# Kernel tuning notes

Measured on AMD Instinct MI355X. Metric: run time of the kernel, lower is better.

Reference implementation:

```python
import jax, jax.numpy as jnp
import numpy as np

N = 50000
E = 600000
D = 128
EPS = 1e-5  # nn.LayerNorm default eps


def gcn_conv(x, W, b, src, dst):
    # PyG GCNConv with add_self_loops=True, edge_weight=None (all ones),
    # symmetric normalization D^-1/2 (A+I) D^-1/2.
    h = x @ W                                        # [N, D]
    deg = jnp.zeros((N,), h.dtype).at[dst].add(1.0) + 1.0  # +1 for self loop
    dinv = jax.lax.rsqrt(deg)                        # deg >= 1, safe
    norm = dinv[src] * dinv[dst]                     # [E]
    msg = h[src] * norm[:, None]                     # [E, D] gather
    agg = jax.ops.segment_sum(msg, dst, num_segments=N)
    agg = agg + h * (dinv * dinv)[:, None]           # self-loop term
    return agg + b


def layer_norm(x, g, b):
    mu = jnp.mean(x, axis=-1, keepdims=True)
    var = jnp.mean(jnp.square(x - mu), axis=-1, keepdims=True)
    return (x - mu) * jax.lax.rsqrt(var + EPS) * g + b


def setup_inputs() -> dict:
    key = jax.random.key(0)
    ks = jax.random.split(key, 6)
    x = jax.random.normal(ks[0], (N, D), dtype=jnp.float32)
    edge_index = jax.random.randint(ks[1], (2, E), 0, N, dtype=jnp.int64)
    s = 1.0 / np.sqrt(D)
    W1 = jax.random.uniform(ks[2], (D, D), jnp.float32, -s, s)
    W2 = jax.random.uniform(ks[3], (D, D), jnp.float32, -s, s)
    b1 = jnp.zeros((D,), jnp.float32)
    b2 = jnp.zeros((D,), jnp.float32)
    ln1_g = jnp.ones((D,), jnp.float32)
    ln1_b = jnp.zeros((D,), jnp.float32)
    ln2_g = jnp.ones((D,), jnp.float32)
    ln2_b = jnp.zeros((D,), jnp.float32)
    return {"x": x, "edge_index": edge_index, "W1": W1, "b1": b1,
            "ln1_g": ln1_g, "ln1_b": ln1_b, "W2": W2, "b2": b2,
            "ln2_g": ln2_g, "ln2_b": ln2_b}


def reference(x, edge_index, W1, b1, ln1_g, ln1_b, W2, b2, ln2_g, ln2_b):
    src, dst = edge_index[0], edge_index[1]
    out = gcn_conv(x, W1, b1, src, dst)
    out = jax.nn.relu(layer_norm(out, ln1_g, ln1_b))  # dropout = identity (eval)
    out = gcn_conv(out, W2, b2, src, dst)
    out = jax.nn.relu(layer_norm(out, ln2_g, ln2_b))
    return out + x
```

## Files before the change

kernel.cpp:

```cpp
#include <hip/hip_runtime.h>
#include <hip/hip_fp16.h>

#define D 128
#define EPS 1e-5f
#define KB 64
#define NBSH 7
#define BUCKW 128

typedef unsigned int u32;
typedef unsigned short u16;
typedef unsigned char u8;
typedef __attribute__((ext_vector_type(8))) _Float16 half8;
typedef __attribute__((ext_vector_type(4))) float f32x4;
typedef __attribute__((ext_vector_type(2))) float f32x2;

__device__ inline u16 f2h(float x) {
  _Float16 t = (_Float16)x;
  return __builtin_bit_cast(u16, t);
}
__device__ inline u8 f2fp8(float x) {
  return (u8)(__builtin_amdgcn_cvt_pk_fp8_f32(x, x, 0, false) & 0xff);
}

__global__ __launch_bounds__(256) void k_prep(const float* __restrict__ W1,
                                              const float* __restrict__ W2,
                                              u16* __restrict__ Wt1,
                                              u16* __restrict__ Wt2) {
  int i = blockIdx.x * 256 + threadIdx.x;
  if (i < 2 * D * D) {
    const float* W = (i < D * D) ? W1 : W2;
    u16* Wt = (i < D * D) ? Wt1 : Wt2;
    int ii = i & (D * D - 1);
    int k = ii >> 7, c = ii & 127;
    Wt[c * D + k] = f2h(W[ii]);
  }
}

template <bool F32IN>
__device__ __forceinline__ void gemm_body(const void* __restrict__ in_,
                                          const u16* __restrict__ Wt,
                                          u8* __restrict__ out, int nrows,
                                          int blk) {
  const int tid = threadIdx.x;
  const int lane = tid & 63, wv = tid >> 6;
  const int m = lane & 15, q = lane >> 4;
  const int r0 = blk * 64 + wv * 16;
  const int rowa = min(r0 + m, nrows - 1);

  f32x4 acc[8];
#pragma unroll
  for (int ct = 0; ct < 8; ct++) acc[ct] = (f32x4)(0.0f);

#pragma unroll
  for (int kk = 0; kk < 4; kk++) {
    const int kbase = kk * 32 + q * 8;
    half8 a;
    if (F32IN) {
      const float* in = (const float*)in_;
      float4 v0 = *(const float4*)(in + (size_t)rowa * D + kbase);
      float4 v1 = *(const float4*)(in + (size_t)rowa * D + kbase + 4);
      a[0] = (_Float16)v0.x; a[1] = (_Float16)v0.y;
      a[2] = (_Float16)v0.z; a[3] = (_Float16)v0.w;
      a[4] = (_Float16)v1.x; a[5] = (_Float16)v1.y;
      a[6] = (_Float16)v1.z; a[7] = (_Float16)v1.w;
    } else {
      const u16* in = (const u16*)in_;
      a = *(const half8*)(in + (size_t)rowa * D + kbase);
    }
#pragma unroll
    for (int ct = 0; ct < 8; ct++) {
      half8 b = *(const half8*)(Wt + (ct * 16 + m) * D + kbase);
      acc[ct] = __builtin_amdgcn_mfma_f32_16x16x32_f16(a, b, acc[ct], 0, 0, 0);
    }
  }

#pragma unroll
  for (int ct = 0; ct < 8; ct++) {
#pragma unroll
    for (int rg = 0; rg < 4; rg++) {
      int rr = r0 + q * 4 + rg;
      if (rr < nrows) out[(size_t)rr * D + ct * 16 + m] = f2fp8(acc[ct][rg]);
    }
  }
}

__global__ __launch_bounds__(256) void k_count_gemm1(
    const int* __restrict__ dst, int* __restrict__ cnt, int E, int NB, int EPB,
    const float* __restrict__ x, const u16* __restrict__ Wt1,
    u8* __restrict__ A, int nrows) {
  if (blockIdx.x < (u32)KB) {
    __shared__ int hist[512];
    const int k = blockIdx.x, tid = threadIdx.x;
    for (int i = tid; i < NB; i += 256) hist[i] = 0;
    __syncthreads();
    const int e0 = k * EPB, e1 = min(E, e0 + EPB);
    for (int base = e0 + tid; base < e1; base += 2048) {
      int dd[8];
#pragma unroll
      for (int i = 0; i < 8; i++) {
        int e = base + i * 256;
        dd[i] = (e < e1) ? dst[e] : -1;
      }
#pragma unroll
      for (int i = 0; i < 8; i++)
        if (dd[i] >= 0) atomicAdd(&hist[dd[i] >> NBSH], 1);
    }
    __syncthreads();
    for (int b = tid; b < NB; b += 256) cnt[b * KB + k] = hist[b];
  } else {
    gemm_body<true>(x, Wt1, A, nrows, blockIdx.x - KB);
  }
}

__global__ __launch_bounds__(256) void k_scan_reduce(
    const int* __restrict__ cnt, int M, int* __restrict__ bsum) {
  const int b = blockIdx.x, t = threadIdx.x;
  const int lane = t & 63, w = t >> 6;
  int idx = b * 1024 + t * 4;
  int4 v = make_int4(0, 0, 0, 0);
  if (idx + 3 < M) {
    v = *(const int4*)(cnt + idx);
  } else {
    if (idx + 0 < M) v.x = cnt[idx + 0];
    if (idx + 1 < M) v.y = cnt[idx + 1];
    if (idx + 2 < M) v.z = cnt[idx + 2];
  }
  int s = v.x + v.y + v.z + v.w;
#pragma unroll
  for (int o = 1; o < 64; o <<= 1) s += __shfl_xor(s, o, 64);
  __shared__ int ws[4];
  if (lane == 0) ws[w] = s;
  __syncthreads();
  if (t == 0) bsum[b] = ws[0] + ws[1] + ws[2] + ws[3];
}

__global__ __launch_bounds__(64) void k_scan_mid(const int* __restrict__ bsum,
                                                 int* __restrict__ boff,
                                                 int SB, int* __restrict__ bsv,
                                                 int NB, int E) {
  const int lane = threadIdx.x;
  int running = 0;
  for (int base = 0; base < SB; base += 64) {
    int i = base + lane;
    int v = (i < SB) ? bsum[i] : 0;
    int incl = v;
#pragma unroll
    for (int o = 1; o < 64; o <<= 1) {
      int t = __shfl_up(incl, o, 64);
      if (lane >= o) incl += t;
    }
    if (i < SB) boff[i] = running + incl - v;
    running += __shfl(incl, 63, 64);
  }
  if (lane == 0) bsv[NB] = E;
}

__global__ __launch_bounds__(256) void k_scan_apply(
    int* __restrict__ cnt, int M, const int* __restrict__ boff,
    int* __restrict__ bsv) {
  const int b = blockIdx.x, t = threadIdx.x;
  const int lane = t & 63, w = t >> 6;
  int idx = b * 1024 + t * 4;
  int4 v = make_int4(0, 0, 0, 0);
  if (idx + 3 < M) {
    v = *(const int4*)(cnt + idx);
  } else {
    if (idx + 0 < M) v.x = cnt[idx + 0];
    if (idx + 1 < M) v.y = cnt[idx + 1];
    if (idx + 2 < M) v.z = cnt[idx + 2];
  }
  int s = v.x + v.y + v.z + v.w;
  int incl = s;
#pragma unroll
  for (int o = 1; o < 64; o <<= 1) {
    int u = __shfl_up(incl, o, 64);
    if (lane >= o) incl += u;
  }
  __shared__ int ws[4];
  if (lane == 63) ws[w] = incl;
  __syncthreads();
  int wbase = 0;
#pragma unroll
  for (int j = 0; j < 4; j++)
    if (j < w) wbase += ws[j];
  int base = boff[b] + wbase + incl - s;
  int e0 = base, e1 = e0 + v.x, e2 = e1 + v.y, e3 = e2 + v.z;
  if (idx < M) {
    cnt[idx] = e0;
    if ((idx & (KB - 1)) == 0) bsv[idx >> 6] = e0;
  }
  if (idx + 1 < M) cnt[idx + 1] = e1;
  if (idx + 2 < M) cnt[idx + 2] = e2;
  if (idx + 3 < M) cnt[idx + 3] = e3;
}

__global__ __launch_bounds__(256) void k_scatter(
    const int* __restrict__ src, const int* __restrict__ dst,
    const int* __restrict__ cnt, u32* __restrict__ tmp, int E, int NB,
    int EPB) {
  __shared__ int off[512];
  const int k = blockIdx.x, tid = threadIdx.x;
  for (int b = tid; b < NB; b += 256) off[b] = cnt[b * KB + k];
  __syncthreads();
  const int e0 = k * EPB, e1 = min(E, e0 + EPB);
  for (int base = e0 + tid; base < e1; base += 2048) {
    int dd[8], ss[8];
#pragma unroll
    for (int i = 0; i < 8; i++) {
      int e = base + i * 256;
      dd[i] = (e < e1) ? dst[e] : -1;
      ss[i] = (e < e1) ? src[e] : 0;
    }
#pragma unroll
    for (int i = 0; i < 8; i++) {
      if (dd[i] >= 0) {
        int p = atomicAdd(&off[dd[i] >> NBSH], 1);
        tmp[p] = (u32)ss[i] | ((u32)(dd[i] & (BUCKW - 1)) << 16);
      }
    }
  }
}

__global__ __launch_bounds__(256) void k_bucket(
    const u32* __restrict__ tmp, const int* __restrict__ bsv,
    int4* __restrict__ meta, float* __restrict__ dinv,
    u32* __restrict__ csr, int N) {
  __shared__ int hist[BUCKW];
  __shared__ int sc[BUCKW];
  __shared__ int cur[BUCKW];
  const int b = blockIdx.x, tid = threadIdx.x;
  const int s0 = bsv[b], s1 = bsv[b + 1];
  if (tid < BUCKW) hist[tid] = 0;
  __syncthreads();
  for (int base = s0 + tid; base < s1; base += 1024) {
    int tt[4];
#pragma unroll
    for (int i = 0; i < 4; i++) {
      int idx = base + i * 256;
      tt[i] = (idx < s1) ? (int)tmp[idx] : -1;
    }
#pragma unroll
    for (int i = 0; i < 4; i++)
      if (tt[i] >= 0) atomicAdd(&hist[(tt[i] >> 16) & (BUCKW - 1)], 1);
  }
  __syncthreads();
  if (tid < BUCKW) sc[tid] = hist[tid];
  __syncthreads();
#pragma unroll
  for (int o = 1; o < BUCKW; o <<= 1) {
    int t = 0;
    if (tid < BUCKW && tid >= o) t = sc[tid - o];
    __syncthreads();
    if (tid < BUCKW) sc[tid] += t;
    __syncthreads();
  }
  if (tid < BUCKW) {
    int dg = hist[tid];
    int excl = sc[tid] - dg;
    cur[tid] = excl;
    int d = (b << NBSH) + tid;
    if (d < N) {
      float dv = rsqrtf((float)dg + 1.0f);
      meta[d] = make_int4(s0 + excl, dg, __builtin_bit_cast(int, dv), 0);
      dinv[d] = dv;
    }
  }
  __syncthreads();
  for (int base = s0 + tid; base < s1; base += 1024) {
    int tt[4];
#pragma unroll
    for (int i = 0; i < 4; i++) {
      int idx = base + i * 256;
      tt[i] = (idx < s1) ? (int)tmp[idx] : -1;
    }
#pragma unroll
    for (int i = 0; i < 4; i++) {
      if (tt[i] >= 0) {
        int r = atomicAdd(&cur[(tt[i] >> 16) & (BUCKW - 1)], 1);
        csr[s0 + r] = (u32)tt[i] & 0xffffu;
      }
    }
  }
}

__global__ __launch_bounds__(256) void k_weights(
    const int4* __restrict__ meta, const float* __restrict__ dinv,
    u32* __restrict__ csr, int N) {
  int gid = blockIdx.x * 256 + threadIdx.x;
  int r = gid >> 2, j0 = gid & 3;
  if (r >= N) return;
  int4 mt = meta[r];
  float dv = __builtin_bit_cast(float, mt.z);
  for (int j = j0; j < mt.y; j += 4) {
    u32 s = csr[mt.x + j];
    float w = dinv[s] * dv;
    csr[mt.x + j] = s | ((u32)f2h(w) << 16);
  }
}

#define ACC_EDGE(vv, ee)                                                     \
  {                                                                          \
    float ww = (float)__builtin_bit_cast(_Float16, (u16)((ee) >> 16));       \
    f32x2 p_;                                                                \
    p_ = __builtin_amdgcn_cvt_pk_f32_fp8(vv.x, false);                       \
    acc[0] = fmaf(p_[0], ww, acc[0]); acc[1] = fmaf(p_[1], ww, acc[1]);      \
    p_ = __builtin_amdgcn_cvt_pk_f32_fp8(vv.x, true);                        \
    acc[2] = fmaf(p_[0], ww, acc[2]); acc[3] = fmaf(p_[1], ww, acc[3]);      \
    p_ = __builtin_amdgcn_cvt_pk_f32_fp8(vv.y, false);                       \
    acc[4] = fmaf(p_[0], ww, acc[4]); acc[5] = fmaf(p_[1], ww, acc[5]);      \
    p_ = __builtin_amdgcn_cvt_pk_f32_fp8(vv.y, true);                        \
    acc[6] = fmaf(p_[0], ww, acc[6]); acc[7] = fmaf(p_[1], ww, acc[7]);      \
  }

__device__ __forceinline__ void gather_ln_core(
    const uint2* __restrict__ hb, const int4* __restrict__ meta,
    const u32* __restrict__ csr, const float* __restrict__ b,
    const float* __restrict__ g, const float* __restrict__ bln,
    int row, int n, int sl, float out[8]) {
  const bool valid = row < n;
  const int rc = valid ? row : 0;
  int4 mt = meta[rc];
  int beg = mt.x;
  int cnt = valid ? mt.y : 0;
  float dv = __builtin_bit_cast(float, mt.z);
  float sn = dv * dv;

  float acc[8];
  {
    uint2 su = hb[(size_t)rc * 16 + sl];
    f32x2 p0 = __builtin_amdgcn_cvt_pk_f32_fp8(su.x, false);
    f32x2 p1 = __builtin_amdgcn_cvt_pk_f32_fp8(su.x, true);
    f32x2 p2 = __builtin_amdgcn_cvt_pk_f32_fp8(su.y, false);
    f32x2 p3 = __builtin_amdgcn_cvt_pk_f32_fp8(su.y, true);
    acc[0] = p0[0] * sn; acc[1] = p0[1] * sn;
    acc[2] = p1[0] * sn; acc[3] = p1[1] * sn;
    acc[4] = p2[0] * sn; acc[5] = p2[1] * sn;
    acc[6] = p3[0] * sn; acc[7] = p3[1] * sn;
  }

  int cm = max(cnt, __shfl_xor(cnt, 16, 64));
  cm = max(cm, __shfl_xor(cm, 32, 64));

  for (int j0 = 0; j0 < cm; j0 += 8) {
    u32 e[8];
#pragma unroll
    for (int jj = 0; jj < 8; jj++) {
      int j = j0 + jj;
      e[jj] = (j < cnt) ? csr[beg + j] : 0u;
    }
    uint2 v[8];
#pragma unroll
    for (int jj = 0; jj < 8; jj++)
      v[jj] = hb[(size_t)(e[jj] & 0xffffu) * 16 + sl];
#pragma unroll
    for (int jj = 0; jj < 8; jj++) ACC_EDGE(v[jj], e[jj]);
  }

  int d0 = sl * 8;
  float4 bb0 = *(const float4*)(b + d0);
  float4 bb1 = *(const float4*)(b + d0 + 4);
  float a0 = acc[0] + bb0.x, a1 = acc[1] + bb0.y;
  float a2 = acc[2] + bb0.z, a3 = acc[3] + bb0.w;
  float a4 = acc[4] + bb1.x, a5 = acc[5] + bb1.y;
  float a6 = acc[6] + bb1.z, a7 = acc[7] + bb1.w;

  float sum = ((a0 + a1) + (a2 + a3)) + ((a4 + a5) + (a6 + a7));
#pragma unroll
  for (int o = 8; o >= 1; o >>= 1) sum += __shfl_xor(sum, o, 16);
  float mu = sum * (1.0f / 128.0f);
  float e0 = a0 - mu, e1 = a1 - mu, e2 = a2 - mu, e3 = a3 - mu;
  float e4 = a4 - mu, e5 = a5 - mu, e6 = a6 - mu, e7 = a7 - mu;
  float vs = ((e0 * e0 + e1 * e1) + (e2 * e2 + e3 * e3)) +
             ((e4 * e4 + e5 * e5) + (e6 * e6 + e7 * e7));
#pragma unroll
  for (int o = 8; o >= 1; o >>= 1) vs += __shfl_xor(vs, o, 16);
  float inv = rsqrtf(vs * (1.0f / 128.0f) + EPS);

  float4 gg0 = *(const float4*)(g + d0);
  float4 gg1 = *(const float4*)(g + d0 + 4);
  float4 bl0 = *(const float4*)(bln + d0);
  float4 bl1 = *(const float4*)(bln + d0 + 4);
  out[0] = fmaxf(e0 * inv * gg0.x + bl0.x, 0.0f);
  out[1] = fmaxf(e1 * inv * gg0.y + bl0.y, 0.0f);
  out[2] = fmaxf(e2 * inv * gg0.z + bl0.z, 0.0f);
  out[3] = fmaxf(e3 * inv * gg0.w + bl0.w, 0.0f);
  out[4] = fmaxf(e4 * inv * gg1.x + bl1.x, 0.0f);
  out[5] = fmaxf(e5 * inv * gg1.y + bl1.y, 0.0f);
  out[6] = fmaxf(e6 * inv * gg1.z + bl1.z, 0.0f);
  out[7] = fmaxf(e7 * inv * gg1.w + bl1.w, 0.0f);
}

__global__ __launch_bounds__(256, 8) void k_gather1(
    const uint2* __restrict__ hb, const int4* __restrict__ meta,
    const u32* __restrict__ csr,
    const float* __restrict__ b, const float* __restrict__ g,
    const float* __restrict__ bln,
    u16* __restrict__ y1, int n) {
  const int tid = threadIdx.x;
  const int sl = tid & 15;
  const int row = blockIdx.x * 16 + (tid >> 4);
  float o[8];
  gather_ln_core(hb, meta, csr, b, g, bln, row, n, sl, o);
  if (row >= n) return;
  uint4 pk;
  pk.x = ((u32)f2h(o[1]) << 16) | (u32)f2h(o[0]);
  pk.y = ((u32)f2h(o[3]) << 16) | (u32)f2h(o[2]);
  pk.z = ((u32)f2h(o[5]) << 16) | (u32)f2h(o[4]);
  pk.w = ((u32)f2h(o[7]) << 16) | (u32)f2h(o[6]);
  *(uint4*)(y1 + (size_t)row * D + sl * 8) = pk;
}

__global__ __launch_bounds__(256) void k_gemm2(const u16* __restrict__ y1,
                                               const u16* __restrict__ Wt2,
                                               u8* __restrict__ outB, int n) {
  gemm_body<false>(y1, Wt2, outB, n, blockIdx.x);
}

__global__ __launch_bounds__(256, 8) void k_gather2(
    const uint2* __restrict__ hb, const int4* __restrict__ meta,
    const u32* __restrict__ csr,
    const float* __restrict__ b, const float* __restrict__ g,
    const float* __restrict__ bln, const float* __restrict__ resid,
    float* __restrict__ outf, int n) {
  const int tid = threadIdx.x;
  const int sl = tid & 15;
  const int row = blockIdx.x * 16 + (tid >> 4);
  float o[8];
  gather_ln_core(hb, meta, csr, b, g, bln, row, n, sl, o);
  if (row >= n) return;
  size_t base = (size_t)row * D + sl * 8;
  float4 r0 = *(const float4*)(resid + base);
  float4 r1 = *(const float4*)(resid + base + 4);
  *(float4*)(outf + base) =
      make_float4(o[0] + r0.x, o[1] + r0.y, o[2] + r0.z, o[3] + r0.w);
  *(float4*)(outf + base + 4) =
      make_float4(o[4] + r1.x, o[5] + r1.y, o[6] + r1.z, o[7] + r1.w);
}

extern "C" void kernel_launch(void* const* d_in, const int* in_sizes, int n_in,
                              void* d_out, int out_size, void* d_ws, size_t ws_size,
                              hipStream_t stream) {
  const float* x    = (const float*)d_in[0];
  const int*   ei   = (const int*)d_in[1];
  const float* W1   = (const float*)d_in[2];
  const float* b1   = (const float*)d_in[3];
  const float* g1   = (const float*)d_in[4];
  const float* bl1  = (const float*)d_in[5];
  const float* W2   = (const float*)d_in[6];
  const float* b2   = (const float*)d_in[7];
  const float* g2   = (const float*)d_in[8];
  const float* bl2  = (const float*)d_in[9];

  const int N = in_sizes[0] / D;
  const int E = in_sizes[1] / 2;
  const int* src = ei;
  const int* dst = ei + E;

  const int NB  = (N + BUCKW - 1) / BUCKW;
  const int M   = NB * KB;
  const int EPB = (E + KB - 1) / KB;
  const int GB  = (N + 63) / 64;
  const int RB  = (N + 15) / 16;
  const int SB  = (M + 1023) / 1024;

  size_t off = 0;
  auto walloc = [&](size_t bytes) {
    void* p = (char*)d_ws + off;
    off = (off + bytes + 255) & ~(size_t)255;
    return p;
  };
  int*   cnt   = (int*)walloc((size_t)M * 4);
  int*   bsum  = (int*)walloc((size_t)SB * 4);
  int*   boff  = (int*)walloc((size_t)SB * 4);
  int*   bsv   = (int*)walloc((size_t)(NB + 1) * 4);
  u32*   tmp   = (u32*)walloc((size_t)E * 4);
  u32*   csr   = (u32*)walloc((size_t)E * 4);
  int4*  meta  = (int4*)walloc((size_t)N * 16);
  float* dinv  = (float*)walloc((size_t)N * 4);
  u8*    A     = (u8*)walloc((size_t)N * D);
  u8*    B     = (u8*)walloc((size_t)N * D);
  u16*   Wt1   = (u16*)walloc((size_t)D * D * 2);
  u16*   Wt2   = (u16*)walloc((size_t)D * D * 2);
  u16*   y1    = (u16*)walloc((size_t)N * D * 2);
  float* O     = (float*)d_out;

  k_prep<<<(2 * D * D + 255) / 256, 256, 0, stream>>>(W1, W2, Wt1, Wt2);
  k_count_gemm1<<<KB + GB, 256, 0, stream>>>(dst, cnt, E, NB, EPB, x, Wt1, A, N);
  k_scan_reduce<<<SB, 256, 0, stream>>>(cnt, M, bsum);
  k_scan_mid<<<1, 64, 0, stream>>>(bsum, boff, SB, bsv, NB, E);
  k_scan_apply<<<SB, 256, 0, stream>>>(cnt, M, boff, bsv);
  k_scatter<<<KB, 256, 0, stream>>>(src, dst, cnt, tmp, E, NB, EPB);
  k_bucket<<<NB, 256, 0, stream>>>(tmp, bsv, meta, dinv, csr, N);
  k_weights<<<(N * 4 + 255) / 256, 256, 0, stream>>>(meta, dinv, csr, N);
  k_gather1<<<RB, 256, 0, stream>>>((const uint2*)A, meta, csr, b1, g1, bl1,
                                    y1, N);
  k_gemm2<<<GB, 256, 0, stream>>>(y1, Wt2, B, N);
  k_gather2<<<RB, 256, 0, stream>>>((const uint2*)B, meta, csr,
                                    b2, g2, bl2, x, O, N);
}
```

Baseline: 193.8 us.

## Compute degrees early, fold edge weights into bucket pass, drop scan_mid and weights kernels

Per-node degrees are now counted with global atomics during the histogram pass, and dinv is computed alongside the scan reduce. This lets the bucket kernel write normalized fp16 edge weights directly into the CSR, removing the separate k_weights pass. The single-block scan_mid kernel is removed by having each scan_apply block sum the preceding block totals itself. The gather loop also prefetches the next batch of CSR entries. The cost is 600k extra global atomics on deg and redundant prefix summation in each scan_apply block, in exchange for two fewer launches and one fewer CSR read-modify-write pass.

New measurement: 205.7 us. 1.06x slower.

```diff
diff --git a/kernel.cpp b/kernel.cpp
--- a/kernel.cpp
+++ b/kernel.cpp
@@ -25,14 +25,18 @@
 __global__ __launch_bounds__(256) void k_prep(const float* __restrict__ W1,
                                               const float* __restrict__ W2,
                                               u16* __restrict__ Wt1,
-                                              u16* __restrict__ Wt2) {
-  int i = blockIdx.x * 256 + threadIdx.x;
-  if (i < 2 * D * D) {
+                                              u16* __restrict__ Wt2,
+                                              int* __restrict__ deg, int N) {
+  if (blockIdx.x < 128) {
+    int i = blockIdx.x * 256 + threadIdx.x;
     const float* W = (i < D * D) ? W1 : W2;
     u16* Wt = (i < D * D) ? Wt1 : Wt2;
     int ii = i & (D * D - 1);
     int k = ii >> 7, c = ii & 127;
     Wt[c * D + k] = f2h(W[ii]);
+  } else {
+    int i = (blockIdx.x - 128) * 256 + threadIdx.x;
+    if (i < N) deg[i] = 0;
   }
 }
 
@@ -85,7 +89,8 @@
 }
 
 __global__ __launch_bounds__(256) void k_count_gemm1(
-    const int* __restrict__ dst, int* __restrict__ cnt, int E, int NB, int EPB,
+    const int* __restrict__ dst, int* __restrict__ cnt, int* __restrict__ deg,
+    int E, int NB, int EPB,
     const float* __restrict__ x, const u16* __restrict__ Wt1,
     u8* __restrict__ A, int nrows) {
   if (blockIdx.x < (u32)KB) {
@@ -103,7 +108,10 @@
       }
 #pragma unroll
       for (int i = 0; i < 8; i++)
-        if (dd[i] >= 0) atomicAdd(&hist[dd[i] >> NBSH], 1);
+        if (dd[i] >= 0) {
+          atomicAdd(&hist[dd[i] >> NBSH], 1);
+          atomicAdd(&deg[dd[i]], 1);
+        }
     }
     __syncthreads();
     for (int b = tid; b < NB; b += 256) cnt[b * KB + k] = hist[b];
@@ -113,7 +121,15 @@
 }
 
 __global__ __launch_bounds__(256) void k_scan_reduce(
-    const int* __restrict__ cnt, int M, int* __restrict__ bsum) {
+    const int* __restrict__ cnt, int M, int* __restrict__ bsum,
+    const int* __restrict__ deg, float* __restrict__ dinv, int N, int SB,
+    int* __restrict__ bsv, int NB, int E) {
+  if ((int)blockIdx.x >= SB) {
+    int i = ((int)blockIdx.x - SB) * 256 + threadIdx.x;
+    if (i < N) dinv[i] = rsqrtf((float)deg[i] + 1.0f);
+    if ((int)blockIdx.x == SB && threadIdx.x == 0) bsv[NB] = E;
+    return;
+  }
   const int b = blockIdx.x, t = threadIdx.x;
   const int lane = t & 63, w = t >> 6;
   int idx = b * 1024 + t * 4;
@@ -134,29 +150,8 @@
   if (t == 0) bsum[b] = ws[0] + ws[1] + ws[2] + ws[3];
 }
 
-__global__ __launch_bounds__(64) void k_scan_mid(const int* __restrict__ bsum,
-                                                 int* __restrict__ boff,
-                                                 int SB, int* __restrict__ bsv,
-                                                 int NB, int E) {
-  const int lane = threadIdx.x;
-  int running = 0;
-  for (int base = 0; base < SB; base += 64) {
-    int i = base + lane;
-    int v = (i < SB) ? bsum[i] : 0;
-    int incl = v;
-#pragma unroll
-    for (int o = 1; o < 64; o <<= 1) {
-      int t = __shfl_up(incl, o, 64);
-      if (lane >= o) incl += t;
-    }
-    if (i < SB) boff[i] = running + incl - v;
-    running += __shfl(incl, 63, 64);
-  }
-  if (lane == 0) bsv[NB] = E;
-}
-
 __global__ __launch_bounds__(256) void k_scan_apply(
-    int* __restrict__ cnt, int M, const int* __restrict__ boff,
+    int* __restrict__ cnt, int M, const int* __restrict__ bsum,
     int* __restrict__ bsv) {
   const int b = blockIdx.x, t = threadIdx.x;
   const int lane = t & 63, w = t >> 6;
@@ -177,13 +172,21 @@
     if (lane >= o) incl += u;
   }
   __shared__ int ws[4];
+  __shared__ int sboff;
   if (lane == 63) ws[w] = incl;
+  if (t < 64) {
+    int partial = 0;
+    for (int j = t; j < b; j += 64) partial += bsum[j];
+#pragma unroll
+    for (int o = 32; o >= 1; o >>= 1) partial += __shfl_xor(partial, o, 64);
+    if (t == 0) sboff = partial;
+  }
   __syncthreads();
   int wbase = 0;
 #pragma unroll
   for (int j = 0; j < 4; j++)
     if (j < w) wbase += ws[j];
-  int base = boff[b] + wbase + incl - s;
+  int base = sboff + wbase + incl - s;
   int e0 = base, e1 = e0 + v.x, e2 = e1 + v.y, e3 = e2 + v.z;
   if (idx < M) {
     cnt[idx] = e0;
@@ -223,14 +226,19 @@
 
 __global__ __launch_bounds__(256) void k_bucket(
     const u32* __restrict__ tmp, const int* __restrict__ bsv,
-    int4* __restrict__ meta, float* __restrict__ dinv,
+    const float* __restrict__ dinv, int4* __restrict__ meta,
     u32* __restrict__ csr, int N) {
   __shared__ int hist[BUCKW];
   __shared__ int sc[BUCKW];
   __shared__ int cur[BUCKW];
+  __shared__ float sdv[BUCKW];
   const int b = blockIdx.x, tid = threadIdx.x;
   const int s0 = bsv[b], s1 = bsv[b + 1];
-  if (tid < BUCKW) hist[tid] = 0;
+  if (tid < BUCKW) {
+    hist[tid] = 0;
+    int d = (b << NBSH) + tid;
+    sdv[tid] = (d < N) ? dinv[d] : 0.0f;
+  }
   __syncthreads();
   for (int base = s0 + tid; base < s1; base += 1024) {
     int tt[4];
@@ -259,11 +267,8 @@
     int excl = sc[tid] - dg;
     cur[tid] = excl;
     int d = (b << NBSH) + tid;
-    if (d < N) {
-      float dv = rsqrtf((float)dg + 1.0f);
-      meta[d] = make_int4(s0 + excl, dg, __builtin_bit_cast(int, dv), 0);
-      dinv[d] = dv;
-    }
+    if (d < N)
+      meta[d] = make_int4(s0 + excl, dg, __builtin_bit_cast(int, sdv[tid]), 0);
   }
   __syncthreads();
   for (int base = s0 + tid; base < s1; base += 1024) {
@@ -273,28 +278,19 @@
       int idx = base + i * 256;
       tt[i] = (idx < s1) ? (int)tmp[idx] : -1;
     }
+    float wsrc[4];
+#pragma unroll
+    for (int i = 0; i < 4; i++)
+      wsrc[i] = (tt[i] >= 0) ? dinv[(u32)tt[i] & 0xffffu] : 0.0f;
 #pragma unroll
     for (int i = 0; i < 4; i++) {
       if (tt[i] >= 0) {
-        int r = atomicAdd(&cur[(tt[i] >> 16) & (BUCKW - 1)], 1);
-        csr[s0 + r] = (u32)tt[i] & 0xffffu;
+        int dl = (tt[i] >> 16) & (BUCKW - 1);
+        int r = atomicAdd(&cur[dl], 1);
+        csr[s0 + r] =
+            ((u32)tt[i] & 0xffffu) | ((u32)f2h(wsrc[i] * sdv[dl]) << 16);
       }
     }
-  }
-}
-
-__global__ __launch_bounds__(256) void k_weights(
-    const int4* __restrict__ meta, const float* __restrict__ dinv,
-    u32* __restrict__ csr, int N) {
-  int gid = blockIdx.x * 256 + threadIdx.x;
-  int r = gid >> 2, j0 = gid & 3;
-  if (r >= N) return;
-  int4 mt = meta[r];
-  float dv = __builtin_bit_cast(float, mt.z);
-  for (int j = j0; j < mt.y; j += 4) {
-    u32 s = csr[mt.x + j];
-    float w = dinv[s] * dv;
-    csr[mt.x + j] = s | ((u32)f2h(w) << 16);
   }
 }
 
@@ -341,19 +337,25 @@
   int cm = max(cnt, __shfl_xor(cnt, 16, 64));
   cm = max(cm, __shfl_xor(cm, 32, 64));
 
+  u32 e[8];
+#pragma unroll
+  for (int jj = 0; jj < 8; jj++)
+    e[jj] = (jj < cnt) ? csr[beg + jj] : 0u;
+
   for (int j0 = 0; j0 < cm; j0 += 8) {
-    u32 e[8];
-#pragma unroll
-    for (int jj = 0; jj < 8; jj++) {
-      int j = j0 + jj;
-      e[jj] = (j < cnt) ? csr[beg + j] : 0u;
-    }
     uint2 v[8];
 #pragma unroll
     for (int jj = 0; jj < 8; jj++)
       v[jj] = hb[(size_t)(e[jj] & 0xffffu) * 16 + sl];
+    u32 en[8];
+    const int jn = j0 + 8;
+#pragma unroll
+    for (int jj = 0; jj < 8; jj++)
+      en[jj] = (jn + jj < cnt) ? csr[beg + jn + jj] : 0u;
 #pragma unroll
     for (int jj = 0; jj < 8; jj++) ACC_EDGE(v[jj], e[jj]);
+#pragma unroll
+    for (int jj = 0; jj < 8; jj++) e[jj] = en[jj];
   }
 
   int d0 = sl * 8;
@@ -462,6 +464,7 @@
   const int GB  = (N + 63) / 64;
   const int RB  = (N + 15) / 16;
   const int SB  = (M + 1023) / 1024;
+  const int ZB  = (N + 255) / 256;
 
   size_t off = 0;
   auto walloc = [&](size_t bytes) {
@@ -471,8 +474,8 @@
   };
   int*   cnt   = (int*)walloc((size_t)M * 4);
   int*   bsum  = (int*)walloc((size_t)SB * 4);
-  int*   boff  = (int*)walloc((size_t)SB * 4);
   int*   bsv   = (int*)walloc((size_t)(NB + 1) * 4);
+  int*   deg   = (int*)walloc((size_t)N * 4);
   u32*   tmp   = (u32*)walloc((size_t)E * 4);
   u32*   csr   = (u32*)walloc((size_t)E * 4);
   int4*  meta  = (int4*)walloc((size_t)N * 16);
@@ -484,14 +487,14 @@
   u16*   y1    = (u16*)walloc((size_t)N * D * 2);
   float* O     = (float*)d_out;
 
-  k_prep<<<(2 * D * D + 255) / 256, 256, 0, stream>>>(W1, W2, Wt1, Wt2);
-  k_count_gemm1<<<KB + GB, 256, 0, stream>>>(dst, cnt, E, NB, EPB, x, Wt1, A, N);
-  k_scan_reduce<<<SB, 256, 0, stream>>>(cnt, M, bsum);
-  k_scan_mid<<<1, 64, 0, stream>>>(bsum, boff, SB, bsv, NB, E);
-  k_scan_apply<<<SB, 256, 0, stream>>>(cnt, M, boff, bsv);
+  k_prep<<<128 + ZB, 256, 0, stream>>>(W1, W2, Wt1, Wt2, deg, N);
+  k_count_gemm1<<<KB + GB, 256, 0, stream>>>(dst, cnt, deg, E, NB, EPB,
+                                             x, Wt1, A, N);
+  k_scan_reduce<<<SB + ZB, 256, 0, stream>>>(cnt, M, bsum, deg, dinv, N, SB,
+                                             bsv, NB, E);
+  k_scan_apply<<<SB, 256, 0, stream>>>(cnt, M, bsum, bsv);
   k_scatter<<<KB, 256, 0, stream>>>(src, dst, cnt, tmp, E, NB, EPB);
-  k_bucket<<<NB, 256, 0, stream>>>(tmp, bsv, meta, dinv, csr, N);
-  k_weights<<<(N * 4 + 255) / 256, 256, 0, stream>>>(meta, dinv, csr, N);
+  k_bucket<<<NB, 256, 0, stream>>>(tmp, bsv, dinv, meta, csr, N);
   k_gather1<<<RB, 256, 0, stream>>>((const uint2*)A, meta, csr, b1, g1, bl1,
                                     y1, N);
   k_gemm2<<<GB, 256, 0, stream>>>(y1, Wt2, B, N);
```

## Sort rows by degree for gather load balance and fold scan-mid into scan-apply

Applied to the files above, without the earlier changes.

Builds a degree histogram in the bucket kernel, scans it, and writes a degree-sorted row permutation in the weights kernel. Both gather kernels now process rows in that order, so the 16 rows sharing a block have similar edge counts and lanes diverge less. Separately, the single-block mid-scan kernel is removed and each scan-apply block sums the preceding block totals itself, which drops one launch. The cost is an extra small kernel, global atomics for the histogram and permutation, and scattered output writes and row accesses in the gathers.

Measured after the change: 359.2 us. 1.85x slower.

```diff
diff --git a/kernel.cpp b/kernel.cpp
--- a/kernel.cpp
+++ b/kernel.cpp
@@ -25,14 +25,17 @@
 __global__ __launch_bounds__(256) void k_prep(const float* __restrict__ W1,
                                               const float* __restrict__ W2,
                                               u16* __restrict__ Wt1,
-                                              u16* __restrict__ Wt2) {
-  int i = blockIdx.x * 256 + threadIdx.x;
-  if (i < 2 * D * D) {
+                                              u16* __restrict__ Wt2,
+                                              int* __restrict__ dhist) {
+  if (blockIdx.x < 128) {
+    int i = blockIdx.x * 256 + threadIdx.x;
     const float* W = (i < D * D) ? W1 : W2;
     u16* Wt = (i < D * D) ? Wt1 : Wt2;
     int ii = i & (D * D - 1);
     int k = ii >> 7, c = ii & 127;
     Wt[c * D + k] = f2h(W[ii]);
+  } else {
+    if (threadIdx.x < 64) dhist[threadIdx.x] = 0;
   }
 }
 
@@ -134,32 +137,12 @@
   if (t == 0) bsum[b] = ws[0] + ws[1] + ws[2] + ws[3];
 }
 
-__global__ __launch_bounds__(64) void k_scan_mid(const int* __restrict__ bsum,
-                                                 int* __restrict__ boff,
-                                                 int SB, int* __restrict__ bsv,
-                                                 int NB, int E) {
-  const int lane = threadIdx.x;
-  int running = 0;
-  for (int base = 0; base < SB; base += 64) {
-    int i = base + lane;
-    int v = (i < SB) ? bsum[i] : 0;
-    int incl = v;
-#pragma unroll
-    for (int o = 1; o < 64; o <<= 1) {
-      int t = __shfl_up(incl, o, 64);
-      if (lane >= o) incl += t;
-    }
-    if (i < SB) boff[i] = running + incl - v;
-    running += __shfl(incl, 63, 64);
-  }
-  if (lane == 0) bsv[NB] = E;
-}
-
 __global__ __launch_bounds__(256) void k_scan_apply(
-    int* __restrict__ cnt, int M, const int* __restrict__ boff,
-    int* __restrict__ bsv) {
+    int* __restrict__ cnt, int M, const int* __restrict__ bsum,
+    int* __restrict__ bsv, int NB, int E) {
   const int b = blockIdx.x, t = threadIdx.x;
   const int lane = t & 63, w = t >> 6;
+  if (b == 0 && t == 0) bsv[NB] = E;
   int idx = b * 1024 + t * 4;
   int4 v = make_int4(0, 0, 0, 0);
   if (idx + 3 < M) {
@@ -177,13 +160,21 @@
     if (lane >= o) incl += u;
   }
   __shared__ int ws[4];
+  __shared__ int sboff;
   if (lane == 63) ws[w] = incl;
+  if (t < 64) {
+    int partial = 0;
+    for (int j = t; j < b; j += 64) partial += bsum[j];
+#pragma unroll
+    for (int o = 32; o >= 1; o >>= 1) partial += __shfl_xor(partial, o, 64);
+    if (t == 0) sboff = partial;
+  }
   __syncthreads();
   int wbase = 0;
 #pragma unroll
   for (int j = 0; j < 4; j++)
     if (j < w) wbase += ws[j];
-  int base = boff[b] + wbase + incl - s;
+  int base = sboff + wbase + incl - s;
   int e0 = base, e1 = e0 + v.x, e2 = e1 + v.y, e3 = e2 + v.z;
   if (idx < M) {
     cnt[idx] = e0;
@@ -224,13 +215,15 @@
 __global__ __launch_bounds__(256) void k_bucket(
     const u32* __restrict__ tmp, const int* __restrict__ bsv,
     int4* __restrict__ meta, float* __restrict__ dinv,
-    u32* __restrict__ csr, int N) {
+    u32* __restrict__ csr, int* __restrict__ dhist, int N) {
   __shared__ int hist[BUCKW];
   __shared__ int sc[BUCKW];
   __shared__ int cur[BUCKW];
+  __shared__ int dh[64];
   const int b = blockIdx.x, tid = threadIdx.x;
   const int s0 = bsv[b], s1 = bsv[b + 1];
   if (tid < BUCKW) hist[tid] = 0;
+  if (tid >= BUCKW && tid < BUCKW + 64) dh[tid - BUCKW] = 0;
   __syncthreads();
   for (int base = s0 + tid; base < s1; base += 1024) {
     int tt[4];
@@ -263,9 +256,11 @@
       float dv = rsqrtf((float)dg + 1.0f);
       meta[d] = make_int4(s0 + excl, dg, __builtin_bit_cast(int, dv), 0);
       dinv[d] = dv;
-    }
-  }
-  __syncthreads();
+      atomicAdd(&dh[min(dg, 63)], 1);
+    }
+  }
+  __syncthreads();
+  if (tid < 64 && dh[tid] > 0) atomicAdd(&dhist[tid], dh[tid]);
   for (int base = s0 + tid; base < s1; base += 1024) {
     int tt[4];
 #pragma unroll
@@ -283,13 +278,31 @@
   }
 }
 
+__global__ __launch_bounds__(64) void k_binscan(const int* __restrict__ dhist,
+                                                int* __restrict__ bincur) {
+  const int t = threadIdx.x;
+  int v = dhist[t];
+  int incl = v;
+#pragma unroll
+  for (int o = 1; o < 64; o <<= 1) {
+    int u = __shfl_up(incl, o, 64);
+    if (t >= o) incl += u;
+  }
+  bincur[t] = incl - v;
+}
+
 __global__ __launch_bounds__(256) void k_weights(
     const int4* __restrict__ meta, const float* __restrict__ dinv,
-    u32* __restrict__ csr, int N) {
+    u32* __restrict__ csr, int* __restrict__ bincur, int* __restrict__ perm,
+    int N) {
   int gid = blockIdx.x * 256 + threadIdx.x;
   int r = gid >> 2, j0 = gid & 3;
   if (r >= N) return;
   int4 mt = meta[r];
+  if (j0 == 0) {
+    int slot = atomicAdd(&bincur[min(mt.y, 63)], 1);
+    perm[slot] = r;
+  }
   float dv = __builtin_bit_cast(float, mt.z);
   for (int j = j0; j < mt.y; j += 4) {
     u32 s = csr[mt.x + j];
@@ -392,16 +405,17 @@
 
 __global__ __launch_bounds__(256, 8) void k_gather1(
     const uint2* __restrict__ hb, const int4* __restrict__ meta,
-    const u32* __restrict__ csr,
+    const u32* __restrict__ csr, const int* __restrict__ perm,
     const float* __restrict__ b, const float* __restrict__ g,
     const float* __restrict__ bln,
     u16* __restrict__ y1, int n) {
   const int tid = threadIdx.x;
   const int sl = tid & 15;
-  const int row = blockIdx.x * 16 + (tid >> 4);
+  const int pr = blockIdx.x * 16 + (tid >> 4);
+  const int row = (pr < n) ? perm[pr] : n;
   float o[8];
   gather_ln_core(hb, meta, csr, b, g, bln, row, n, sl, o);
-  if (row >= n) return;
+  if (pr >= n) return;
   uint4 pk;
   pk.x = ((u32)f2h(o[1]) << 16) | (u32)f2h(o[0]);
   pk.y = ((u32)f2h(o[3]) << 16) | (u32)f2h(o[2]);
@@ -418,16 +432,17 @@
 
 __global__ __launch_bounds__(256, 8) void k_gather2(
     const uint2* __restrict__ hb, const int4* __restrict__ meta,
-    const u32* __restrict__ csr,
+    const u32* __restrict__ csr, const int* __restrict__ perm,
     const float* __restrict__ b, const float* __restrict__ g,
     const float* __restrict__ bln, const float* __restrict__ resid,
     float* __restrict__ outf, int n) {
   const int tid = threadIdx.x;
   const int sl = tid & 15;
-  const int row = blockIdx.x * 16 + (tid >> 4);
+  const int pr = blockIdx.x * 16 + (tid >> 4);
+  const int row = (pr < n) ? perm[pr] : n;
   float o[8];
   gather_ln_core(hb, meta, csr, b, g, bln, row, n, sl, o);
-  if (row >= n) return;
+  if (pr >= n) return;
   size_t base = (size_t)row * D + sl * 8;
   float4 r0 = *(const float4*)(resid + base);
   float4 r1 = *(const float4*)(resid + base + 4);
@@ -471,8 +486,10 @@
   };
   int*   cnt   = (int*)walloc((size_t)M * 4);
   int*   bsum  = (int*)walloc((size_t)SB * 4);
-  int*   boff  = (int*)walloc((size_t)SB * 4);
   int*   bsv   = (int*)walloc((size_t)(NB + 1) * 4);
+  int*   dhist = (int*)walloc(64 * 4);
+  int*   bincur= (int*)walloc(64 * 4);
+  int*   perm  = (int*)walloc((size_t)N * 4);
   u32*   tmp   = (u32*)walloc((size_t)E * 4);
   u32*   csr   = (u32*)walloc((size_t)E * 4);
   int4*  meta  = (int4*)walloc((size_t)N * 16);
@@ -484,17 +501,18 @@
   u16*   y1    = (u16*)walloc((size_t)N * D * 2);
   float* O     = (float*)d_out;
 
-  k_prep<<<(2 * D * D + 255) / 256, 256, 0, stream>>>(W1, W2, Wt1, Wt2);
+  k_prep<<<129, 256, 0, stream>>>(W1, W2, Wt1, Wt2, dhist);
   k_count_gemm1<<<KB + GB, 256, 0, stream>>>(dst, cnt, E, NB, EPB, x, Wt1, A, N);
   k_scan_reduce<<<SB, 256, 0, stream>>>(cnt, M, bsum);
-  k_scan_mid<<<1, 64, 0, stream>>>(bsum, boff, SB, bsv, NB, E);
-  k_scan_apply<<<SB, 256, 0, stream>>>(cnt, M, boff, bsv);
+  k_scan_apply<<<SB, 256, 0, stream>>>(cnt, M, bsum, bsv, NB, E);
   k_scatter<<<KB, 256, 0, stream>>>(src, dst, cnt, tmp, E, NB, EPB);
-  k_bucket<<<NB, 256, 0, stream>>>(tmp, bsv, meta, dinv, csr, N);
-  k_weights<<<(N * 4 + 255) / 256, 256, 0, stream>>>(meta, dinv, csr, N);
-  k_gather1<<<RB, 256, 0, stream>>>((const uint2*)A, meta, csr, b1, g1, bl1,
-                                    y1, N);
+  k_bucket<<<NB, 256, 0, stream>>>(tmp, bsv, meta, dinv, csr, dhist, N);
+  k_binscan<<<1, 64, 0, stream>>>(dhist, bincur);
+  k_weights<<<(N * 4 + 255) / 256, 256, 0, stream>>>(meta, dinv, csr, bincur,
+                                                     perm, N);
+  k_gather1<<<RB, 256, 0, stream>>>((const uint2*)A, meta, csr, perm,
+                                    b1, g1, bl1, y1, N);
   k_gemm2<<<GB, 256, 0, stream>>>(y1, Wt2, B, N);
-  k_gather2<<<RB, 256, 0, stream>>>((const uint2*)B, meta, csr,
+  k_gather2<<<RB, 256, 0, stream>>>((const uint2*)B, meta, csr, perm,
                                     b2, g2, bl2, x, O, N);
 }
```

## Split CSR neighbors by source half, fold scan-mid into apply, nontemporal output

Applied to the files above, without the earlier changes.

Removes the single-block k_scan_mid launch: each k_scan_apply block now sums the preceding block totals itself to get its offset. k_bucket partitions each row's neighbor list into sources in the lower and upper halves of the node range and stores the split count in meta.w. The gather loops then process the two halves in separate phases, aiming for better cache locality of the feature gathers. The final output uses nontemporal loads and stores. The costs are a redundant O(SB) reduction in every scan block and an extra divergence-padded loop per row in the gathers.

Result: no change. 195.4 us (+0.8%).

```diff
diff --git a/kernel.cpp b/kernel.cpp
--- a/kernel.cpp
+++ b/kernel.cpp
@@ -134,32 +134,12 @@
   if (t == 0) bsum[b] = ws[0] + ws[1] + ws[2] + ws[3];
 }
 
-__global__ __launch_bounds__(64) void k_scan_mid(const int* __restrict__ bsum,
-                                                 int* __restrict__ boff,
-                                                 int SB, int* __restrict__ bsv,
-                                                 int NB, int E) {
-  const int lane = threadIdx.x;
-  int running = 0;
-  for (int base = 0; base < SB; base += 64) {
-    int i = base + lane;
-    int v = (i < SB) ? bsum[i] : 0;
-    int incl = v;
-#pragma unroll
-    for (int o = 1; o < 64; o <<= 1) {
-      int t = __shfl_up(incl, o, 64);
-      if (lane >= o) incl += t;
-    }
-    if (i < SB) boff[i] = running + incl - v;
-    running += __shfl(incl, 63, 64);
-  }
-  if (lane == 0) bsv[NB] = E;
-}
-
 __global__ __launch_bounds__(256) void k_scan_apply(
-    int* __restrict__ cnt, int M, const int* __restrict__ boff,
-    int* __restrict__ bsv) {
+    int* __restrict__ cnt, int M, const int* __restrict__ bsum,
+    int* __restrict__ bsv, int NB, int E) {
   const int b = blockIdx.x, t = threadIdx.x;
   const int lane = t & 63, w = t >> 6;
+  if (b == 0 && t == 0) bsv[NB] = E;
   int idx = b * 1024 + t * 4;
   int4 v = make_int4(0, 0, 0, 0);
   if (idx + 3 < M) {
@@ -177,13 +157,21 @@
     if (lane >= o) incl += u;
   }
   __shared__ int ws[4];
+  __shared__ int sboff;
   if (lane == 63) ws[w] = incl;
+  if (t < 64) {
+    int partial = 0;
+    for (int j = t; j < b; j += 64) partial += bsum[j];
+#pragma unroll
+    for (int o = 32; o >= 1; o >>= 1) partial += __shfl_xor(partial, o, 64);
+    if (t == 0) sboff = partial;
+  }
   __syncthreads();
   int wbase = 0;
 #pragma unroll
   for (int j = 0; j < 4; j++)
     if (j < w) wbase += ws[j];
-  int base = boff[b] + wbase + incl - s;
+  int base = sboff + wbase + incl - s;
   int e0 = base, e1 = e0 + v.x, e2 = e1 + v.y, e3 = e2 + v.z;
   if (idx < M) {
     cnt[idx] = e0;
@@ -224,10 +212,11 @@
 __global__ __launch_bounds__(256) void k_bucket(
     const u32* __restrict__ tmp, const int* __restrict__ bsv,
     int4* __restrict__ meta, float* __restrict__ dinv,
-    u32* __restrict__ csr, int N) {
+    u32* __restrict__ csr, int N, int SLAB) {
   __shared__ int hist[BUCKW];
   __shared__ int sc[BUCKW];
-  __shared__ int cur[BUCKW];
+  __shared__ int curlo[BUCKW];
+  __shared__ int curhi[BUCKW];
   const int b = blockIdx.x, tid = threadIdx.x;
   const int s0 = bsv[b], s1 = bsv[b + 1];
   if (tid < BUCKW) hist[tid] = 0;
@@ -257,7 +246,8 @@
   if (tid < BUCKW) {
     int dg = hist[tid];
     int excl = sc[tid] - dg;
-    cur[tid] = excl;
+    curlo[tid] = excl;
+    curhi[tid] = excl + dg - 1;
     int d = (b << NBSH) + tid;
     if (d < N) {
       float dv = rsqrtf((float)dg + 1.0f);
@@ -276,9 +266,20 @@
 #pragma unroll
     for (int i = 0; i < 4; i++) {
       if (tt[i] >= 0) {
-        int r = atomicAdd(&cur[(tt[i] >> 16) & (BUCKW - 1)], 1);
-        csr[s0 + r] = (u32)tt[i] & 0xffffu;
+        int dl = (tt[i] >> 16) & (BUCKW - 1);
+        int sr = (int)((u32)tt[i] & 0xffffu);
+        int r = (sr < SLAB) ? atomicAdd(&curlo[dl], 1)
+                            : atomicSub(&curhi[dl], 1);
+        csr[s0 + r] = (u32)sr;
       }
+    }
+  }
+  __syncthreads();
+  if (tid < BUCKW) {
+    int d = (b << NBSH) + tid;
+    if (d < N) {
+      int excl = sc[tid] - hist[tid];
+      ((int*)meta)[d * 4 + 3] = curlo[tid] - excl;
     }
   }
 }
@@ -322,6 +323,7 @@
   int4 mt = meta[rc];
   int beg = mt.x;
   int cnt = valid ? mt.y : 0;
+  int c0 = valid ? mt.w : 0;
   float dv = __builtin_bit_cast(float, mt.z);
   float sn = dv * dv;
 
@@ -338,15 +340,33 @@
     acc[6] = p3[0] * sn; acc[7] = p3[1] * sn;
   }
 
-  int cm = max(cnt, __shfl_xor(cnt, 16, 64));
-  cm = max(cm, __shfl_xor(cm, 32, 64));
-
-  for (int j0 = 0; j0 < cm; j0 += 8) {
+  int cm0 = max(c0, __shfl_xor(c0, 16, 64));
+  cm0 = max(cm0, __shfl_xor(cm0, 32, 64));
+  for (int j0 = 0; j0 < cm0; j0 += 8) {
     u32 e[8];
 #pragma unroll
     for (int jj = 0; jj < 8; jj++) {
       int j = j0 + jj;
-      e[jj] = (j < cnt) ? csr[beg + j] : 0u;
+      e[jj] = (j < c0) ? csr[beg + j] : 0u;
+    }
+    uint2 v[8];
+#pragma unroll
+    for (int jj = 0; jj < 8; jj++)
+      v[jj] = hb[(size_t)(e[jj] & 0xffffu) * 16 + sl];
+#pragma unroll
+    for (int jj = 0; jj < 8; jj++) ACC_EDGE(v[jj], e[jj]);
+  }
+
+  int c1 = cnt - c0;
+  int cm1 = max(c1, __shfl_xor(c1, 16, 64));
+  cm1 = max(cm1, __shfl_xor(cm1, 32, 64));
+  const int b1 = beg + c0;
+  for (int j0 = 0; j0 < cm1; j0 += 8) {
+    u32 e[8];
+#pragma unroll
+    for (int jj = 0; jj < 8; jj++) {
+      int j = j0 + jj;
+      e[jj] = (j < c1) ? csr[b1 + j] : 0u;
     }
     uint2 v[8];
 #pragma unroll
@@ -429,12 +449,15 @@
   gather_ln_core(hb, meta, csr, b, g, bln, row, n, sl, o);
   if (row >= n) return;
   size_t base = (size_t)row * D + sl * 8;
-  float4 r0 = *(const float4*)(resid + base);
-  float4 r1 = *(const float4*)(resid + base + 4);
-  *(float4*)(outf + base) =
-      make_float4(o[0] + r0.x, o[1] + r0.y, o[2] + r0.z, o[3] + r0.w);
-  *(float4*)(outf + base + 4) =
-      make_float4(o[4] + r1.x, o[5] + r1.y, o[6] + r1.z, o[7] + r1.w);
+  f32x4 r0 = __builtin_nontemporal_load((const f32x4*)(resid + base));
+  f32x4 r1 = __builtin_nontemporal_load((const f32x4*)(resid + base + 4));
+  f32x4 w0, w1;
+  w0[0] = o[0] + r0[0]; w0[1] = o[1] + r0[1];
+  w0[2] = o[2] + r0[2]; w0[3] = o[3] + r0[3];
+  w1[0] = o[4] + r1[0]; w1[1] = o[5] + r1[1];
+  w1[2] = o[6] + r1[2]; w1[3] = o[7] + r1[3];
+  __builtin_nontemporal_store(w0, (f32x4*)(outf + base));
+  __builtin_nontemporal_store(w1, (f32x4*)(outf + base + 4));
 }
 
 extern "C" void kernel_launch(void* const* d_in, const int* in_sizes, int n_in,
@@ -462,6 +485,7 @@
   const int GB  = (N + 63) / 64;
   const int RB  = (N + 15) / 16;
   const int SB  = (M + 1023) / 1024;
+  const int SLAB = (N + 1) / 2;
 
   size_t off = 0;
   auto walloc = [&](size_t bytes) {
@@ -471,7 +495,6 @@
   };
   int*   cnt   = (int*)walloc((size_t)M * 4);
   int*   bsum  = (int*)walloc((size_t)SB * 4);
-  int*   boff  = (int*)walloc((size_t)SB * 4);
   int*   bsv   = (int*)walloc((size_t)(NB + 1) * 4);
   u32*   tmp   = (u32*)walloc((size_t)E * 4);
   u32*   csr   = (u32*)walloc((size_t)E * 4);
@@ -487,10 +510,9 @@
   k_prep<<<(2 * D * D + 255) / 256, 256, 0, stream>>>(W1, W2, Wt1, Wt2);
   k_count_gemm1<<<KB + GB, 256, 0, stream>>>(dst, cnt, E, NB, EPB, x, Wt1, A, N);
   k_scan_reduce<<<SB, 256, 0, stream>>>(cnt, M, bsum);
-  k_scan_mid<<<1, 64, 0, stream>>>(bsum, boff, SB, bsv, NB, E);
-  k_scan_apply<<<SB, 256, 0, stream>>>(cnt, M, boff, bsv);
+  k_scan_apply<<<SB, 256, 0, stream>>>(cnt, M, bsum, bsv, NB, E);
   k_scatter<<<KB, 256, 0, stream>>>(src, dst, cnt, tmp, E, NB, EPB);
-  k_bucket<<<NB, 256, 0, stream>>>(tmp, bsv, meta, dinv, csr, N);
+  k_bucket<<<NB, 256, 0, stream>>>(tmp, bsv, meta, dinv, csr, N, SLAB);
   k_weights<<<(N * 4 + 255) / 256, 256, 0, stream>>>(meta, dinv, csr, N);
   k_gather1<<<RB, 256, 0, stream>>>((const uint2*)A, meta, csr, b1, g1, bl1,
                                     y1, N);
```
